# Kernel optimization log

Hardware: AMD Instinct MI355X
Metric: run time of the kernel (lower is better)

The kernel has to match this reference:

```python
import jax, jax.numpy as jnp
import numpy as np


def _nn_sq_dists(query, ref):
    # query: [B, N, 3], ref: [B, M, 3]
    # squared distance via ||q||^2 + ||r||^2 - 2 q.r, min over ref points
    q2 = jnp.sum(query * query, axis=-1)            # [B, N]
    r2 = jnp.sum(ref * ref, axis=-1)                # [B, M]
    cross = jnp.einsum('bnc,bmc->bnm', query, ref)  # [B, N, M]
    d = q2[:, :, None] + r2[:, None, :] - 2.0 * cross
    d = jnp.maximum(d, 0.0)  # clamp numerical negatives (true distances >= 0)
    return jnp.min(d, axis=-1)                      # [B, N] 1-NN squared dists


def setup_inputs() -> dict:
    key = jax.random.key(0)
    k1, k2 = jax.random.split(key)
    B, C, N = 4, 3, 8192
    pc2 = jax.random.normal(k1, (B, C, N), dtype=jnp.float32)
    pc1_warped = jax.random.normal(k2, (B, C, N), dtype=jnp.float32)
    return {"pc2": pc2, "pc1_warped": pc1_warped}


def reference(pc2, pc1_warped):
    # pos1 = target['pc2'], pos2 = output['pc1_warped'], both [B, 3, N]
    pos1 = jnp.transpose(pc2, (0, 2, 1))         # [B, N, 3]
    pos2 = jnp.transpose(pc1_warped, (0, 2, 1))  # [B, N, 3]
    # pointutils.knn(1, pos1, pos2): for each pos1 point, nearest in pos2.
    nn_d = _nn_sq_dists(pos1, pos2)              # [B, N]
    per_batch = jnp.sum(nn_d, axis=1)            # sum over dim 1
    loss = per_batch.mean() + per_batch.mean()
    return loss
```

## Files before the change

### kernel.cpp

```cpp
#include <hip/hip_runtime.h>


#define NPTS    8192
#define NB      4
#define TOTQ    (NB * NPTS)
#define BQ      256
#define QT      4
#define QPB     (BQ * QT)
#define MC      512
#define MCHUNKS (NPTS / MC)

__global__ __launch_bounds__(BQ) void chamfer_partial(
    const float* __restrict__ pc2,
    const float* __restrict__ pc1w,
    float* __restrict__ partial)
{
    __shared__ float4 lds[MC];
    const int tid = threadIdx.x;
    const int b  = blockIdx.z;
    const int m0 = blockIdx.y * MC;
    const int q0 = blockIdx.x * QPB;

    const float* refb = pc1w + b * 3 * NPTS;
    for (int i = tid; i < MC; i += BQ) {
        float rx = refb[m0 + i];
        float ry = refb[NPTS + m0 + i];
        float rz = refb[2 * NPTS + m0 + i];
        float h  = -0.5f * (rx * rx + ry * ry + rz * rz);
        lds[i] = make_float4(rx, ry, rz, h);
    }
    __syncthreads();

    const float* qb = pc2 + b * 3 * NPTS;
    float qx[QT], qy[QT], qz[QT], smax[QT];
#pragma unroll
    for (int j = 0; j < QT; ++j) {
        int q = q0 + tid + j * BQ;
        qx[j] = qb[q];
        qy[j] = qb[NPTS + q];
        qz[j] = qb[2 * NPTS + q];
        smax[j] = -1e30f;
    }

#pragma unroll 4
    for (int m = 0; m < MC; ++m) {
        float4 r = lds[m];
#pragma unroll
        for (int j = 0; j < QT; ++j) {
            float s = fmaf(qx[j], r.x, r.w);
            s = fmaf(qy[j], r.y, s);
            s = fmaf(qz[j], r.z, s);
            smax[j] = fmaxf(smax[j], s);
        }
    }

#pragma unroll
    for (int j = 0; j < QT; ++j) {
        int q = q0 + tid + j * BQ;
        partial[blockIdx.y * TOTQ + b * NPTS + q] = smax[j];
    }
}

__global__ __launch_bounds__(256) void chamfer_reduce(
    const float* __restrict__ pc2,
    const float* __restrict__ partial,
    float* __restrict__ out)
{
    const int g = blockIdx.x * blockDim.x + threadIdx.x;
    float smax = -1e30f;
#pragma unroll
    for (int c = 0; c < MCHUNKS; ++c)
        smax = fmaxf(smax, partial[c * TOTQ + g]);

    const int b = g / NPTS;
    const int n = g & (NPTS - 1);
    const float* qb = pc2 + b * 3 * NPTS;
    float qx = qb[n], qy = qb[NPTS + n], qz = qb[2 * NPTS + n];
    float q2 = qx * qx + qy * qy + qz * qz;
    float d = fmaxf(q2 - 2.0f * smax, 0.0f);

#pragma unroll
    for (int off = 32; off > 0; off >>= 1)
        d += __shfl_down(d, off, 64);

    __shared__ float wsum[4];
    const int lane = threadIdx.x & 63;
    const int wid  = threadIdx.x >> 6;
    if (lane == 0) wsum[wid] = d;
    __syncthreads();
    if (threadIdx.x == 0) {
        float s = wsum[0] + wsum[1] + wsum[2] + wsum[3];
        atomicAdd(out, s * (2.0f / NB));
    }
}

extern "C" void kernel_launch(void* const* d_in, const int* in_sizes, int n_in,
                              void* d_out, int out_size, void* d_ws, size_t ws_size,
                              hipStream_t stream) {
    const float* pc2  = (const float*)d_in[0];
    const float* pc1w = (const float*)d_in[1];
    float* out = (float*)d_out;
    float* partial = (float*)d_ws;

    dim3 g1(NPTS / QPB, MCHUNKS, NB);
    chamfer_partial<<<g1, BQ, 0, stream>>>(pc2, pc1w, partial);

    hipMemsetAsync(out, 0, sizeof(float), stream);
    chamfer_reduce<<<TOTQ / 256, 256, 0, stream>>>(pc2, partial, out);
}
```

Measured before the change: 84.13 us.

## Use packed float2 FMA for query tiles and halve reference chunk size

Each thread now holds 8 queries as four 2-wide vectors and computes the scores with packed FMA and max operations (v_pk_fma_f32 on CDNA3/4), so one instruction does the work of two scalar FMAs. The reference chunk per block drops from 512 to 256 points so the block grid stays large enough despite the doubled queries per block. The cost is twice as many partial chunks to write and reduce. The reduce kernel still loops over MCHUNKS, so it follows the new value automatically. Packed max may not lower to a packed instruction and could become scalar ops.

```diff
diff --git a/kernel.cpp b/kernel.cpp
--- a/kernel.cpp
+++ b/kernel.cpp
@@ -5,10 +5,25 @@
 #define NB      4
 #define TOTQ    (NB * NPTS)
 #define BQ      256
-#define QT      4
-#define QPB     (BQ * QT)
-#define MC      512
+#define QV      4
+#define QPB     (BQ * QV * 2)
+#define MC      256
 #define MCHUNKS (NPTS / MC)
+
+typedef float v2f __attribute__((ext_vector_type(2)));
+
+#if __has_builtin(__builtin_elementwise_fma)
+#define VFMA(a, b, c) __builtin_elementwise_fma((a), (b), (c))
+#else
+#define VFMA(a, b, c) ((a) * (b) + (c))
+#endif
+#if __has_builtin(__builtin_elementwise_max)
+#define VMAX(a, b) __builtin_elementwise_max((a), (b))
+#else
+static __device__ inline v2f VMAX(v2f a, v2f b) {
+    v2f r; r.x = fmaxf(a.x, b.x); r.y = fmaxf(a.y, b.y); return r;
+}
+#endif
 
 __global__ __launch_bounds__(BQ) void chamfer_partial(
     const float* __restrict__ pc2,
@@ -22,7 +37,8 @@
     const int q0 = blockIdx.x * QPB;
 
     const float* refb = pc1w + b * 3 * NPTS;
-    for (int i = tid; i < MC; i += BQ) {
+    if (tid < MC) {
+        int i = tid;
         float rx = refb[m0 + i];
         float ry = refb[NPTS + m0 + i];
         float rz = refb[2 * NPTS + m0 + i];
@@ -32,32 +48,34 @@
     __syncthreads();
 
     const float* qb = pc2 + b * 3 * NPTS;
-    float qx[QT], qy[QT], qz[QT], smax[QT];
+    v2f qx[QV], qy[QV], qz[QV], smax[QV];
 #pragma unroll
-    for (int j = 0; j < QT; ++j) {
-        int q = q0 + tid + j * BQ;
-        qx[j] = qb[q];
-        qy[j] = qb[NPTS + q];
-        qz[j] = qb[2 * NPTS + q];
-        smax[j] = -1e30f;
+    for (int j = 0; j < QV; ++j) {
+        int off = q0 + j * 2 * BQ;
+        qx[j] = ((const v2f*)(qb + off))[tid];
+        qy[j] = ((const v2f*)(qb + NPTS + off))[tid];
+        qz[j] = ((const v2f*)(qb + 2 * NPTS + off))[tid];
+        smax[j] = (v2f){-1e30f, -1e30f};
     }
 
 #pragma unroll 4
     for (int m = 0; m < MC; ++m) {
         float4 r = lds[m];
+        v2f rx = {r.x, r.x}, ry = {r.y, r.y}, rz = {r.z, r.z}, rw = {r.w, r.w};
 #pragma unroll
-        for (int j = 0; j < QT; ++j) {
-            float s = fmaf(qx[j], r.x, r.w);
-            s = fmaf(qy[j], r.y, s);
-            s = fmaf(qz[j], r.z, s);
-            smax[j] = fmaxf(smax[j], s);
+        for (int j = 0; j < QV; ++j) {
+            v2f s = VFMA(qx[j], rx, rw);
+            s = VFMA(qy[j], ry, s);
+            s = VFMA(qz[j], rz, s);
+            smax[j] = VMAX(smax[j], s);
         }
     }
 
+    float* pbase = partial + blockIdx.y * TOTQ + b * NPTS;
 #pragma unroll
-    for (int j = 0; j < QT; ++j) {
-        int q = q0 + tid + j * BQ;
-        partial[blockIdx.y * TOTQ + b * NPTS + q] = smax[j];
+    for (int j = 0; j < QV; ++j) {
+        int off = q0 + j * 2 * BQ;
+        ((v2f*)(pbase + off))[tid] = smax[j];
     }
 }
 
```

Result: faster. 81.34 us (-3.3%).

## Use packed fp32 FMA with paired references and drop memset launch

Applied to the files above, without the earlier changes.

The distance inner loop now uses two-wide float vectors. Each query value is broadcast and combined with a pair of reference points per packed FMA, which targets the v_pk_fma_f32 instruction on CDNA. The reference LDS layout is interleaved into pairs. Queries per thread grow to 8 while the reference chunk shrinks to 256, and query loads and partial stores become float4. The output memset is folded into the first kernel and the reduce block is widened to 512 threads, which saves a launch but adds more partial chunks and relies on ordering between the two kernels.

```diff
diff --git a/kernel.cpp b/kernel.cpp
--- a/kernel.cpp
+++ b/kernel.cpp
@@ -5,74 +5,108 @@
 #define NB      4
 #define TOTQ    (NB * NPTS)
 #define BQ      256
-#define QT      4
+#define QT      8
 #define QPB     (BQ * QT)
-#define MC      512
+#define MC      256
+#define MP      (MC / 2)
 #define MCHUNKS (NPTS / MC)
+
+typedef float v2f __attribute__((ext_vector_type(2)));
+
+#if __has_builtin(__builtin_elementwise_fma)
+#define VFMA(a, b, c) __builtin_elementwise_fma((a), (b), (c))
+#else
+#define VFMA(a, b, c) ((a) * (b) + (c))
+#endif
 
 __global__ __launch_bounds__(BQ) void chamfer_partial(
     const float* __restrict__ pc2,
     const float* __restrict__ pc1w,
-    float* __restrict__ partial)
+    float* __restrict__ partial,
+    float* __restrict__ out)
 {
-    __shared__ float4 lds[MC];
+    __shared__ v2f lds[MP * 4];
     const int tid = threadIdx.x;
     const int b  = blockIdx.z;
     const int m0 = blockIdx.y * MC;
     const int q0 = blockIdx.x * QPB;
 
+    if (blockIdx.x == 0 && blockIdx.y == 0 && blockIdx.z == 0 && tid == 0)
+        out[0] = 0.0f;
+
     const float* refb = pc1w + b * 3 * NPTS;
-    for (int i = tid; i < MC; i += BQ) {
+    {
+        int i = tid;
         float rx = refb[m0 + i];
         float ry = refb[NPTS + m0 + i];
         float rz = refb[2 * NPTS + m0 + i];
         float h  = -0.5f * (rx * rx + ry * ry + rz * rz);
-        lds[i] = make_float4(rx, ry, rz, h);
+        float* lf = (float*)lds;
+        int base = (i >> 1) * 8 + (i & 1);
+        lf[base + 0] = rx;
+        lf[base + 2] = ry;
+        lf[base + 4] = rz;
+        lf[base + 6] = h;
     }
     __syncthreads();
 
     const float* qb = pc2 + b * 3 * NPTS;
-    float qx[QT], qy[QT], qz[QT], smax[QT];
+    v2f qx2[QT], qy2[QT], qz2[QT];
+    float smax[QT];
 #pragma unroll
-    for (int j = 0; j < QT; ++j) {
-        int q = q0 + tid + j * BQ;
-        qx[j] = qb[q];
-        qy[j] = qb[NPTS + q];
-        qz[j] = qb[2 * NPTS + q];
-        smax[j] = -1e30f;
+    for (int g4 = 0; g4 < 2; ++g4) {
+        int off = q0 + g4 * (BQ * 4);
+        float4 fx = ((const float4*)(qb + off))[tid];
+        float4 fy = ((const float4*)(qb + NPTS + off))[tid];
+        float4 fz = ((const float4*)(qb + 2 * NPTS + off))[tid];
+        int j = g4 * 4;
+        qx2[j+0] = (v2f){fx.x, fx.x}; qx2[j+1] = (v2f){fx.y, fx.y};
+        qx2[j+2] = (v2f){fx.z, fx.z}; qx2[j+3] = (v2f){fx.w, fx.w};
+        qy2[j+0] = (v2f){fy.x, fy.x}; qy2[j+1] = (v2f){fy.y, fy.y};
+        qy2[j+2] = (v2f){fy.z, fy.z}; qy2[j+3] = (v2f){fy.w, fy.w};
+        qz2[j+0] = (v2f){fz.x, fz.x}; qz2[j+1] = (v2f){fz.y, fz.y};
+        qz2[j+2] = (v2f){fz.z, fz.z}; qz2[j+3] = (v2f){fz.w, fz.w};
     }
+#pragma unroll
+    for (int j = 0; j < QT; ++j) smax[j] = -1e30f;
 
-#pragma unroll 4
-    for (int m = 0; m < MC; ++m) {
-        float4 r = lds[m];
+#pragma unroll 2
+    for (int p = 0; p < MP; ++p) {
+        v2f rx = lds[p * 4 + 0];
+        v2f ry = lds[p * 4 + 1];
+        v2f rz = lds[p * 4 + 2];
+        v2f rh = lds[p * 4 + 3];
 #pragma unroll
         for (int j = 0; j < QT; ++j) {
-            float s = fmaf(qx[j], r.x, r.w);
-            s = fmaf(qy[j], r.y, s);
-            s = fmaf(qz[j], r.z, s);
-            smax[j] = fmaxf(smax[j], s);
+            v2f s = VFMA(qx2[j], rx, rh);
+            s = VFMA(qy2[j], ry, s);
+            s = VFMA(qz2[j], rz, s);
+            smax[j] = fmaxf(smax[j], fmaxf(s[0], s[1]));
         }
     }
 
+    float* pbase = partial + blockIdx.y * TOTQ + b * NPTS;
 #pragma unroll
-    for (int j = 0; j < QT; ++j) {
-        int q = q0 + tid + j * BQ;
-        partial[blockIdx.y * TOTQ + b * NPTS + q] = smax[j];
+    for (int g4 = 0; g4 < 2; ++g4) {
+        int off = q0 + g4 * (BQ * 4);
+        int j = g4 * 4;
+        float4 o = make_float4(smax[j], smax[j+1], smax[j+2], smax[j+3]);
+        ((float4*)(pbase + off))[tid] = o;
     }
 }
 
-__global__ __launch_bounds__(256) void chamfer_reduce(
+__global__ __launch_bounds__(512) void chamfer_reduce(
     const float* __restrict__ pc2,
     const float* __restrict__ partial,
     float* __restrict__ out)
 {
-    const int g = blockIdx.x * blockDim.x + threadIdx.x;
+    const int g = blockIdx.x * 512 + threadIdx.x;
     float smax = -1e30f;
 #pragma unroll
     for (int c = 0; c < MCHUNKS; ++c)
         smax = fmaxf(smax, partial[c * TOTQ + g]);
 
-    const int b = g / NPTS;
+    const int b = g >> 13;
     const int n = g & (NPTS - 1);
     const float* qb = pc2 + b * 3 * NPTS;
     float qx = qb[n], qy = qb[NPTS + n], qz = qb[2 * NPTS + n];
@@ -83,13 +117,15 @@
     for (int off = 32; off > 0; off >>= 1)
         d += __shfl_down(d, off, 64);
 
-    __shared__ float wsum[4];
+    __shared__ float wsum[8];
     const int lane = threadIdx.x & 63;
     const int wid  = threadIdx.x >> 6;
     if (lane == 0) wsum[wid] = d;
     __syncthreads();
     if (threadIdx.x == 0) {
-        float s = wsum[0] + wsum[1] + wsum[2] + wsum[3];
+        float s = 0.0f;
+#pragma unroll
+        for (int w = 0; w < 8; ++w) s += wsum[w];
         atomicAdd(out, s * (2.0f / NB));
     }
 }
@@ -103,8 +139,6 @@
     float* partial = (float*)d_ws;
 
     dim3 g1(NPTS / QPB, MCHUNKS, NB);
-    chamfer_partial<<<g1, BQ, 0, stream>>>(pc2, pc1w, partial);
-
-    hipMemsetAsync(out, 0, sizeof(float), stream);
-    chamfer_reduce<<<TOTQ / 256, 256, 0, stream>>>(pc2, partial, out);
+    chamfer_partial<<<g1, BQ, 0, stream>>>(pc2, pc1w, partial, out);
+    chamfer_reduce<<<TOTQ / 512, 512, 0, stream>>>(pc2, partial, out);
 }
```

Result: faster. 80.13 us (-4.8%).

## Compute nearest-neighbor dot products with split-bf16 MFMA instead of scalar FMAs

Applied to the files above, without the earlier changes.

Adds a prep kernel that splits query and reference coordinates (and the -0.5*|r|^2 term) into hi/lo bf16 pairs, packed into MFMA fragment layout. The main kernel then uses 32x32x16 bf16 MFMA to compute query·ref + h for 32x32 tiles and max-reduces them in registers, replacing the scalar fp32 FMA loop. The memset is folded into the prep kernel and the reduction is reshaped for the new partial layout. Accuracy relies on the hi/lo split giving near-fp32 dot products, and the extra prep launch and fragment traffic are added costs.

```diff
diff --git a/kernel.cpp b/kernel.cpp
--- a/kernel.cpp
+++ b/kernel.cpp
@@ -1,79 +1,128 @@
 #include <hip/hip_runtime.h>
 
 
-#define NPTS    8192
-#define NB      4
-#define TOTQ    (NB * NPTS)
-#define BQ      256
-#define QT      4
-#define QPB     (BQ * QT)
-#define MC      512
-#define MCHUNKS (NPTS / MC)
+#define NPTS  8192
+#define NB    4
+#define NCH   256
+#define RR    8
+#define RCPR  32
+#define QPB   4
 
-__global__ __launch_bounds__(BQ) void chamfer_partial(
+typedef float f32x16 __attribute__((ext_vector_type(16)));
+typedef short bf16x8 __attribute__((ext_vector_type(8)));
+
+static __device__ __forceinline__ unsigned int f2bf(float f) {
+    unsigned int u = __float_as_uint(f);
+    u += 0x7FFF + ((u >> 16) & 1);
+    return u >> 16;
+}
+static __device__ __forceinline__ float bf2f(unsigned int s) {
+    return __uint_as_float(s << 16);
+}
+
+__global__ __launch_bounds__(256) void chamfer_prep(
     const float* __restrict__ pc2,
     const float* __restrict__ pc1w,
+    uint4* __restrict__ qfrag, uint4* __restrict__ rfrag,
+    float* __restrict__ out)
+{
+    int t = blockIdx.x * 256 + threadIdx.x;
+    if (t == 0) out[0] = 0.0f;
+    int side = t >> 15;
+    int rem  = t & 32767;
+    int b = rem >> 13;
+    int n = rem & 8191;
+    const float* src = (side ? pc1w : pc2) + b * 3 * NPTS;
+    float x = src[n], y = src[NPTS + n], z = src[2 * NPTS + n];
+    unsigned int xh = f2bf(x), yh = f2bf(y), zh = f2bf(z);
+    unsigned int xl = f2bf(x - bf2f(xh));
+    unsigned int yl = f2bf(y - bf2f(yh));
+    unsigned int zl = f2bf(z - bf2f(zh));
+    int chunk = n >> 5, lane = n & 31;
+    uint4 g0, g1;
+    if (side == 0) {
+        g0.x = xh | (xh << 16);
+        g0.y = xl | (yh << 16);
+        g0.z = yh | (yl << 16);
+        g0.w = zh | (zh << 16);
+        g1.x = zl | (0x3F80u << 16);
+        g1.y = 0x3F80u;
+        g1.z = 0u; g1.w = 0u;
+    } else {
+        float h = -0.5f * (x * x + y * y + z * z);
+        unsigned int hh = f2bf(h);
+        unsigned int hl = f2bf(h - bf2f(hh));
+        g0.x = xh | (xl << 16);
+        g0.y = xh | (yh << 16);
+        g0.z = yl | (yh << 16);
+        g0.w = zh | (zl << 16);
+        g1.x = zh | (hh << 16);
+        g1.y = hl;
+        g1.z = 0u; g1.w = 0u;
+    }
+    uint4* dst = (side ? rfrag : qfrag) + ((b * NCH + chunk) * 64 + lane);
+    dst[0]  = g0;
+    dst[32] = g1;
+}
+
+__global__ __launch_bounds__(256) void chamfer_mfma(
+    const uint4* __restrict__ qfrag, const uint4* __restrict__ rfrag,
     float* __restrict__ partial)
 {
-    __shared__ float4 lds[MC];
-    const int tid = threadIdx.x;
-    const int b  = blockIdx.z;
-    const int m0 = blockIdx.y * MC;
-    const int q0 = blockIdx.x * QPB;
+    __shared__ uint4 slds[2048];
+    const int tid  = threadIdx.x;
+    const int b    = blockIdx.z;
+    const int rr   = blockIdx.y;
+    const int wave = tid >> 6;
+    const int lane = tid & 63;
 
-    const float* refb = pc1w + b * 3 * NPTS;
-    for (int i = tid; i < MC; i += BQ) {
-        float rx = refb[m0 + i];
-        float ry = refb[NPTS + m0 + i];
-        float rz = refb[2 * NPTS + m0 + i];
-        float h  = -0.5f * (rx * rx + ry * ry + rz * rz);
-        lds[i] = make_float4(rx, ry, rz, h);
-    }
+    const uint4* rsrc = rfrag + (b * NCH + rr * RCPR) * 64;
+#pragma unroll
+    for (int i = 0; i < 8; ++i)
+        slds[tid + i * 256] = rsrc[tid + i * 256];
     __syncthreads();
 
-    const float* qb = pc2 + b * 3 * NPTS;
-    float qx[QT], qy[QT], qz[QT], smax[QT];
+    const int qc = blockIdx.x * QPB + wave;
+    uint4 bq_u = qfrag[(b * NCH + qc) * 64 + (lane >> 5) * 32 + (lane & 31)];
+    bf16x8 bq = __builtin_bit_cast(bf16x8, bq_u);
+
+    f32x16 zero;
 #pragma unroll
-    for (int j = 0; j < QT; ++j) {
-        int q = q0 + tid + j * BQ;
-        qx[j] = qb[q];
-        qy[j] = qb[NPTS + q];
-        qz[j] = qb[2 * NPTS + q];
-        smax[j] = -1e30f;
+    for (int i = 0; i < 16; ++i) zero[i] = 0.0f;
+
+    float rm0 = -3e38f, rm1 = -3e38f, rm2 = -3e38f, rm3 = -3e38f;
+    const int abase = (lane >> 5) * 32 + (lane & 31);
+#pragma unroll 2
+    for (int c = 0; c < RCPR; ++c) {
+        bf16x8 a = __builtin_bit_cast(bf16x8, slds[c * 64 + abase]);
+        f32x16 d = __builtin_amdgcn_mfma_f32_32x32x16_bf16(a, bq, zero, 0, 0, 0);
+        rm0 = fmaxf(rm0, fmaxf(d[0],  d[1]));
+        rm0 = fmaxf(rm0, fmaxf(d[2],  d[3]));
+        rm1 = fmaxf(rm1, fmaxf(d[4],  d[5]));
+        rm1 = fmaxf(rm1, fmaxf(d[6],  d[7]));
+        rm2 = fmaxf(rm2, fmaxf(d[8],  d[9]));
+        rm2 = fmaxf(rm2, fmaxf(d[10], d[11]));
+        rm3 = fmaxf(rm3, fmaxf(d[12], d[13]));
+        rm3 = fmaxf(rm3, fmaxf(d[14], d[15]));
     }
-
-#pragma unroll 4
-    for (int m = 0; m < MC; ++m) {
-        float4 r = lds[m];
-#pragma unroll
-        for (int j = 0; j < QT; ++j) {
-            float s = fmaf(qx[j], r.x, r.w);
-            s = fmaf(qy[j], r.y, s);
-            s = fmaf(qz[j], r.z, s);
-            smax[j] = fmaxf(smax[j], s);
-        }
-    }
-
-#pragma unroll
-    for (int j = 0; j < QT; ++j) {
-        int q = q0 + tid + j * BQ;
-        partial[blockIdx.y * TOTQ + b * NPTS + q] = smax[j];
-    }
+    float rm = fmaxf(fmaxf(rm0, rm1), fmaxf(rm2, rm3));
+    rm = fmaxf(rm, __shfl_xor(rm, 32, 64));
+    if (lane < 32)
+        partial[(b * RR + rr) * NPTS + qc * 32 + lane] = rm;
 }
 
-__global__ __launch_bounds__(256) void chamfer_reduce(
+__global__ __launch_bounds__(512) void chamfer_reduce(
     const float* __restrict__ pc2,
     const float* __restrict__ partial,
     float* __restrict__ out)
 {
-    const int g = blockIdx.x * blockDim.x + threadIdx.x;
-    float smax = -1e30f;
+    const int g = blockIdx.x * 512 + threadIdx.x;
+    const int b = g >> 13, n = g & 8191;
+    float smax = -3e38f;
 #pragma unroll
-    for (int c = 0; c < MCHUNKS; ++c)
-        smax = fmaxf(smax, partial[c * TOTQ + g]);
+    for (int c = 0; c < RR; ++c)
+        smax = fmaxf(smax, partial[(b * RR + c) * NPTS + n]);
 
-    const int b = g / NPTS;
-    const int n = g & (NPTS - 1);
     const float* qb = pc2 + b * 3 * NPTS;
     float qx = qb[n], qy = qb[NPTS + n], qz = qb[2 * NPTS + n];
     float q2 = qx * qx + qy * qy + qz * qz;
@@ -83,13 +132,15 @@
     for (int off = 32; off > 0; off >>= 1)
         d += __shfl_down(d, off, 64);
 
-    __shared__ float wsum[4];
+    __shared__ float wsum[8];
     const int lane = threadIdx.x & 63;
     const int wid  = threadIdx.x >> 6;
     if (lane == 0) wsum[wid] = d;
     __syncthreads();
     if (threadIdx.x == 0) {
-        float s = wsum[0] + wsum[1] + wsum[2] + wsum[3];
+        float s = 0.0f;
+#pragma unroll
+        for (int w = 0; w < 8; ++w) s += wsum[w];
         atomicAdd(out, s * (2.0f / NB));
     }
 }
@@ -100,11 +151,12 @@
     const float* pc2  = (const float*)d_in[0];
     const float* pc1w = (const float*)d_in[1];
     float* out = (float*)d_out;
-    float* partial = (float*)d_ws;
+    uint4* qfrag   = (uint4*)d_ws;
+    uint4* rfrag   = (uint4*)((char*)d_ws + (1u << 20));
+    float* partial = (float*)((char*)d_ws + (2u << 20));
 
-    dim3 g1(NPTS / QPB, MCHUNKS, NB);
-    chamfer_partial<<<g1, BQ, 0, stream>>>(pc2, pc1w, partial);
-
-    hipMemsetAsync(out, 0, sizeof(float), stream);
-    chamfer_reduce<<<TOTQ / 256, 256, 0, stream>>>(pc2, partial, out);
+    chamfer_prep<<<256, 256, 0, stream>>>(pc2, pc1w, qfrag, rfrag, out);
+    dim3 g1(NCH / QPB, RR, NB);
+    chamfer_mfma<<<g1, 256, 0, stream>>>(qfrag, rfrag, partial);
+    chamfer_reduce<<<NB * NPTS / 512, 512, 0, stream>>>(pc2, partial, out);
 }
```

Result: faster. 78.99 us (-6.1%).
